# Kernel tuning notes

Measured on AMD Instinct MI355X. Metric: run time of the kernel, lower is better.

Reference implementation:

```python
import jax, jax.numpy as jnp
import numpy as np

ALPHA = 0.2  # LeakyReLU negative slope


def setup_inputs() -> dict:
    key = jax.random.key(0)
    k1, k2, k3, k4 = jax.random.split(key, 4)
    bs, n, fin = 8, 1024, 256
    heads, fo = 8, 64
    h = jax.random.normal(k1, (bs, n, fin), dtype=jnp.float32)
    adj = jax.random.randint(k2, (bs, n, n), 0, 2, dtype=jnp.int32)
    # W stored as [in_features, heads*out] so Wh = h @ W (same math as torch Linear)
    W = jax.random.normal(k3, (fin, heads * fo), dtype=jnp.float32) * 0.1
    a = jax.random.normal(k4, (heads, 2 * fo), dtype=jnp.float32) * 0.1
    return {"h": h, "adj": adj, "W": W, "a": a}


def reference(h, adj, W, a):
    bs, n, _ = h.shape
    heads, two_fo = a.shape
    fo = two_fo // 2
    # Wh: [bs, n, heads, fo]
    Wh = (h @ W).reshape(bs, n, heads, fo)
    a_src, a_dst = a[:, :fo], a[:, fo:]
    # Additive attention decomposed: e[b,h,i,j] = leaky_relu(src[b,h,i] + dst[b,h,j])
    e_src = jnp.einsum('bnhf,hf->bhn', Wh, a_src)  # [bs, heads, n]
    e_dst = jnp.einsum('bnhf,hf->bhn', Wh, a_dst)
    e = e_src[:, :, :, None] + e_dst[:, :, None, :]  # [bs, heads, n, n]
    e = jnp.where(e > 0, e, ALPHA * e)  # LeakyReLU
    e = jnp.where(adj[:, None, :, :] == 0, -jnp.inf, e)
    attn = jax.nn.softmax(e, axis=-1)  # [bs, heads, n, n]
    # h_prime[b,i,h,f] = sum_j attn[b,h,i,j] * Wh[b,j,h,f]
    h_prime = jnp.einsum('bhij,bjhf->bihf', attn, Wh)
    return h_prime.reshape(bs, n, heads * fo)
```

## Files before the change

kernel.cpp:

```cpp
#include <hip/hip_runtime.h>
#include <hip/hip_bf16.h>
#include <math.h>

#define BS 8
#define NN 1024
#define FIN 256
#define HEADS 8
#define FO 64
#define NH (HEADS*FO)
static constexpr float ALPHA = 0.2f;
static constexpr float LOG2E = 1.4426950408889634f;

typedef short bf16x8 __attribute__((ext_vector_type(8)));
typedef float f32x4  __attribute__((ext_vector_type(4)));
typedef unsigned short u16;
typedef unsigned u32;
typedef u16 u16x4v __attribute__((ext_vector_type(4)));
typedef u16 u16x8v __attribute__((ext_vector_type(8)));

__device__ __forceinline__ u16 f2b(float x) {
    __hip_bfloat16 b = __float2bfloat16(x);
    return *reinterpret_cast<u16*>(&b);
}
__device__ __forceinline__ float fexp2(float x) {
#if __has_builtin(__builtin_amdgcn_exp2f)
    return __builtin_amdgcn_exp2f(x);
#else
    float r; asm("v_exp_f32 %0, %1" : "=v"(r) : "v"(x)); return r;
#endif
}
__device__ __forceinline__ void gload_lds16(const void* g, void* l) {
    __builtin_amdgcn_global_load_lds(
        (const __attribute__((address_space(1))) unsigned int*)g,
        (__attribute__((address_space(3))) unsigned int*)l, 16, 0, 0);
}

__global__ __launch_bounds__(256) void prep_misc(const float* __restrict__ h,
                                                 const int* __restrict__ adj,
                                                 const float* __restrict__ W,
                                                 u16* __restrict__ hb,
                                                 u16* __restrict__ WbT,
                                                 u32* __restrict__ bits) {
    const int bid = blockIdx.x;
    const int t = threadIdx.x;
    if (bid < 8192) {
        const int lane = t & 63;
        const size_t e0 = ((size_t)bid * 256 + t) * 4;
        const int4 v = *reinterpret_cast<const int4*>(adj + e0);
        u32 x = (v.x ? 1u : 0u) | (v.y ? 2u : 0u) | (v.z ? 4u : 0u) | (v.w ? 8u : 0u);
        {   const u32 r = (u32)__shfl_xor((int)x, 1);
            const int sh = (lane & 1) * 4;  x = (x << sh) | (r << (4 - sh)); }
        {   const u32 r = (u32)__shfl_xor((int)x, 2);
            const int sh = (lane & 2) * 4;  x = (x << sh) | (r << (8 - sh)); }
        {   const u32 r = (u32)__shfl_xor((int)x, 4);
            const int sh = (lane & 4) * 4;  x = (x << sh) | (r << (16 - sh)); }
        if ((lane & 7) == 0) bits[e0 >> 5] = x;
    } else if (bid < 9216) {
        const int i = ((bid - 8192) * 256 + t) * 8;
        const float4 v0 = *reinterpret_cast<const float4*>(h + i);
        const float4 v1 = *reinterpret_cast<const float4*>(h + i + 4);
        u16x8v o;
        o[0]=f2b(v0.x); o[1]=f2b(v0.y); o[2]=f2b(v0.z); o[3]=f2b(v0.w);
        o[4]=f2b(v1.x); o[5]=f2b(v1.y); o[6]=f2b(v1.z); o[7]=f2b(v1.w);
        *reinterpret_cast<u16x8v*>(hb + i) = o;
    } else {
        __shared__ float T[64][65];
        const int bb = bid - 9216;
        const int hh = bb & 7;
        const int n0 = hh * 64, k0 = (bb >> 3) * 64;
        const int r4 = t >> 6, c = t & 63;
        #pragma unroll
        for (int p = 0; p < 16; ++p) {
            const int r = p * 4 + r4;
            T[r][c] = W[(size_t)(k0 + r) * NH + n0 + c];
        }
        __syncthreads();
        #pragma unroll
        for (int p = 0; p < 16; ++p) {
            const int r = p * 4 + r4;
            WbT[(size_t)(n0 + r) * FIN + k0 + c] = f2b(T[c][r]);
        }
    }
}

__global__ __launch_bounds__(256) void gemm_whT(const u16* __restrict__ hb,
                                                const u16* __restrict__ WbT,
                                                const float* __restrict__ avec,
                                                u16* __restrict__ WhT,
                                                float* __restrict__ esrc,
                                                float* __restrict__ edst) {
    __shared__ u16 Al[2][64 * 64];
    __shared__ u16 Bl[2][64 * 64];
    const int t = threadIdx.x, wv = t >> 6, lane = t & 63;
    const int g = lane >> 4, l15 = lane & 15;
    const int lid = (blockIdx.x & 7) * 128 + (blockIdx.x >> 3);
    const int m0 = (lid >> 3) * 64;
    const int h  = lid & 7;
    const int lr = lane >> 3;
    const int sch = (lane & 7) ^ lr;
    const int bh = (m0 >> 10) * HEADS + h;

    f32x4 acc[4] = {};

    auto stageA = [&](int buf, int k0) {
        #pragma unroll
        for (int c = 0; c < 2; ++c) {
            const int rowb = wv * 16 + c * 8;
            gload_lds16(hb + (size_t)(m0 + rowb + lr) * FIN + k0 + sch * 8,
                        &Al[buf][rowb * 64]);
        }
    };
    auto stageB = [&](int buf, int k0) {
        #pragma unroll
        for (int c = 0; c < 2; ++c) {
            const int rowb = wv * 16 + c * 8;
            gload_lds16(WbT + (size_t)(h * 64 + rowb + lr) * FIN + k0 + sch * 8,
                        &Bl[buf][rowb * 64]);
        }
    };

    stageA(0, 0); stageB(0, 0);
    __syncthreads();
    for (int kt = 0; kt < 4; ++kt) {
        const int buf = kt & 1;
        if (kt < 3) { stageA(buf ^ 1, (kt + 1) * 64); stageB(buf ^ 1, (kt + 1) * 64); }
        #pragma unroll
        for (int ks = 0; ks < 2; ++ks) {
            const int ch = (ks * 4 + g) ^ (l15 & 7);
            const bf16x8 afr = *reinterpret_cast<const bf16x8*>(
                &Al[buf][(wv * 16 + l15) * 64 + ch * 8]);
            #pragma unroll
            for (int n = 0; n < 4; ++n) {
                const bf16x8 bfr = *reinterpret_cast<const bf16x8*>(
                    &Bl[buf][(n * 16 + l15) * 64 + ch * 8]);
                acc[n] = __builtin_amdgcn_mfma_f32_16x16x32_bf16(afr, bfr, acc[n], 0, 0, 0);
            }
        }
        __syncthreads();
    }

    {
        float as_[4], ad_[4];
        #pragma unroll
        for (int n = 0; n < 4; ++n) {
            as_[n] = avec[h * 128 + n * 16 + l15] * LOG2E;
            ad_[n] = avec[h * 128 + 64 + n * 16 + l15] * LOG2E;
        }
        #pragma unroll
        for (int r = 0; r < 4; ++r) {
            float ps = acc[0][r] * as_[0] + acc[1][r] * as_[1]
                     + acc[2][r] * as_[2] + acc[3][r] * as_[3];
            float pd = acc[0][r] * ad_[0] + acc[1][r] * ad_[1]
                     + acc[2][r] * ad_[2] + acc[3][r] * ad_[3];
            #pragma unroll
            for (int off = 1; off < 16; off <<= 1) {
                ps += __shfl_xor(ps, off);
                pd += __shfl_xor(pd, off);
            }
            if (l15 == 0) {
                const int i = (m0 + wv * 16 + g * 4 + r) & (NN - 1);
                esrc[(size_t)bh * NN + i] = ps;
                edst[(size_t)bh * NN + i] = pd;
            }
        }
    }

    u16* scr = &Al[0][0];
    #pragma unroll
    for (int n = 0; n < 4; ++n) {
        u16x4v pk;
        #pragma unroll
        for (int r = 0; r < 4; ++r) pk[r] = f2b(acc[n][r]);
        *reinterpret_cast<u16x4v*>(&scr[(n * 16 + l15) * 72 + wv * 16 + g * 4]) = pk;
    }
    __syncthreads();
    const int il0 = m0 & (NN - 1);
    const int f = t >> 2, q = t & 3;
    const u16x8v v0 = *reinterpret_cast<const u16x8v*>(&scr[f * 72 + q * 16]);
    const u16x8v v1 = *reinterpret_cast<const u16x8v*>(&scr[f * 72 + q * 16 + 8]);
    u16* dst = &WhT[((size_t)bh * 64 + f) * NN + il0 + q * 16];
    *reinterpret_cast<u16x8v*>(dst)     = v0;
    *reinterpret_cast<u16x8v*>(dst + 8) = v1;
}

__global__ __launch_bounds__(128, 4) void attn_pv(const u32* __restrict__ bits,
                                                  const u16* __restrict__ WhT,
                                                  const float* __restrict__ esrc,
                                                  const float* __restrict__ edst,
                                                  float* __restrict__ out) {
    __shared__ u16 Bs[2][64 * 64];
    const int t = threadIdx.x, wv = t >> 6, lane = t & 63;
    const int g = lane >> 4, l15 = lane & 15;
    const int lr = lane >> 3, sch = (lane & 7) ^ lr;

    const int lid = (blockIdx.x & 7) * 256 + (blockIdx.x >> 3);
    const int it = lid & 31, h = (lid >> 5) & 7, b = lid >> 8;
    const int i0 = it * 32;
    const int bh = b * HEADS + h;
    const int rowi = i0 + wv * 16 + l15;

    const float es = esrc[(size_t)bh * NN + rowi];
    const u16*  whb = WhT + (size_t)bh * 64 * NN;
    const float* ed = edst + (size_t)bh * NN + 8 * g;
    const u32*  bitrow = bits + (size_t)(b * NN + rowi) * 32;

    auto stageB = [&](int buf, int j0) {
        #pragma unroll
        for (int c = 0; c < 4; ++c) {
            const int fb = wv * 32 + c * 8;
            gload_lds16(whb + (size_t)(fb + lr) * NN + j0 + sch * 8,
                        &Bs[buf][fb * 64]);
        }
    };

    stageB(0, 0);
    float4 pe0 = *(const float4*)(ed);
    float4 pe1 = *(const float4*)(ed + 4);
    u32    pw  = bitrow[0];
    __syncthreads();

    f32x4 acc[4] = {};
    f32x4 dsum = {};
    bf16x8 ones;
    #pragma unroll
    for (int q = 0; q < 8; ++q) ones[q] = (short)0x3F80;

    for (int tt = 0; tt < 16; ++tt) {
        const int buf = tt & 1;
        if (tt < 15) stageB(buf ^ 1, (tt + 1) * 64);
        #pragma unroll
        for (int ks = 0; ks < 2; ++ks) {
            const int s = tt * 2 + ks;
            const float4 e0 = pe0, e1 = pe1;
            const u32 word = pw;
            if (s < 31) {
                pe0 = *(const float4*)(ed + (s + 1) * 32);
                pe1 = *(const float4*)(ed + (s + 1) * 32 + 4);
                pw  = bitrow[s + 1];
            }
            const int chb = ((ks * 4 + g) ^ (l15 & 7)) * 8;
            const bf16x8 v0 = *(const bf16x8*)(&Bs[buf][(0 * 16 + l15) * 64 + chb]);
            const bf16x8 v1 = *(const bf16x8*)(&Bs[buf][(1 * 16 + l15) * 64 + chb]);
            const bf16x8 v2 = *(const bf16x8*)(&Bs[buf][(2 * 16 + l15) * 64 + chb]);
            const bf16x8 v3 = *(const bf16x8*)(&Bs[buf][(3 * 16 + l15) * 64 + chb]);

            const u32 byte_ = (word >> (8 * g)) & 0xffu;
            float ps[8];
            {
                float sv;
                sv = es + e0.x; sv = fmaxf(sv, ALPHA * sv); sv = (byte_ & 1u)        ? sv : -1e30f; ps[0] = fexp2(sv);
                sv = es + e0.y; sv = fmaxf(sv, ALPHA * sv); sv = ((byte_ >> 1) & 1u) ? sv : -1e30f; ps[1] = fexp2(sv);
                sv = es + e0.z; sv = fmaxf(sv, ALPHA * sv); sv = ((byte_ >> 2) & 1u) ? sv : -1e30f; ps[2] = fexp2(sv);
                sv = es + e0.w; sv = fmaxf(sv, ALPHA * sv); sv = ((byte_ >> 3) & 1u) ? sv : -1e30f; ps[3] = fexp2(sv);
                sv = es + e1.x; sv = fmaxf(sv, ALPHA * sv); sv = ((byte_ >> 4) & 1u) ? sv : -1e30f; ps[4] = fexp2(sv);
                sv = es + e1.y; sv = fmaxf(sv, ALPHA * sv); sv = ((byte_ >> 5) & 1u) ? sv : -1e30f; ps[5] = fexp2(sv);
                sv = es + e1.z; sv = fmaxf(sv, ALPHA * sv); sv = ((byte_ >> 6) & 1u) ? sv : -1e30f; ps[6] = fexp2(sv);
                sv = es + e1.w; sv = fmaxf(sv, ALPHA * sv); sv = ((byte_ >> 7) & 1u) ? sv : -1e30f; ps[7] = fexp2(sv);
            }
            union { u32 u[4]; bf16x8 v; } af;
            #pragma unroll
            for (int qp = 0; qp < 4; ++qp) {
                union { __hip_bfloat162 b2; u32 w; } cv;
                cv.b2 = __float22bfloat162_rn(make_float2(ps[2*qp], ps[2*qp+1]));
                af.u[qp] = cv.w;
            }
            acc[0] = __builtin_amdgcn_mfma_f32_16x16x32_bf16(af.v, v0, acc[0], 0, 0, 0);
            acc[1] = __builtin_amdgcn_mfma_f32_16x16x32_bf16(af.v, v1, acc[1], 0, 0, 0);
            acc[2] = __builtin_amdgcn_mfma_f32_16x16x32_bf16(af.v, v2, acc[2], 0, 0, 0);
            acc[3] = __builtin_amdgcn_mfma_f32_16x16x32_bf16(af.v, v3, acc[3], 0, 0, 0);
            dsum   = __builtin_amdgcn_mfma_f32_16x16x32_bf16(af.v, ones, dsum, 0, 0, 0);
        }
        if (tt < 15) __syncthreads();
    }

    float inv[4];
    #pragma unroll
    for (int r = 0; r < 4; ++r) inv[r] = 1.0f / dsum[r];
    #pragma unroll
    for (int n = 0; n < 4; ++n)
        #pragma unroll
        for (int r = 0; r < 4; ++r) {
            const int io = i0 + wv * 16 + g * 4 + r;
            out[(size_t)(b * NN + io) * NH + h * 64 + n * 16 + l15] =
                acc[n][r] * inv[r];
        }
}

extern "C" void kernel_launch(void* const* d_in, const int* in_sizes, int n_in,
                              void* d_out, int out_size, void* d_ws, size_t ws_size,
                              hipStream_t stream) {
    const float* h   = (const float*)d_in[0];
    const int*   adj = (const int*)  d_in[1];
    const float* W   = (const float*)d_in[2];
    const float* a   = (const float*)d_in[3];
    float* out = (float*)d_out;

    char* p = (char*)d_ws;
    u16*   hb   = (u16*)p;   p += (size_t)BS * NN * FIN * 2;
    u16*   WbT  = (u16*)p;   p += (size_t)NH * FIN * 2;
    u16*   WhT  = (u16*)p;   p += (size_t)BS * HEADS * FO * NN * 2;
    float* esrc = (float*)p; p += (size_t)BS * HEADS * NN * 4;
    float* edst = (float*)p; p += (size_t)BS * HEADS * NN * 4;
    u32*   bits = (u32*)p;

    prep_misc<<<9248, 256, 0, stream>>>(h, adj, W, hb, WbT, bits);
    gemm_whT <<<1024, 256, 0, stream>>>(hb, WbT, a, WhT, esrc, edst);
    attn_pv  <<<2048, 128, 0, stream>>>(bits, WhT, esrc, edst, out);
}
```

Before: 53.34 us.

## Deepen prefetch of edge scores and mask bits, relax barrier waitcnt, raise MFMA priority

```diff
diff --git a/kernel.cpp b/kernel.cpp
--- a/kernel.cpp
+++ b/kernel.cpp
@@ -214,9 +214,14 @@
     };
 
     stageB(0, 0);
-    float4 pe0 = *(const float4*)(ed);
-    float4 pe1 = *(const float4*)(ed + 4);
-    u32    pw  = bitrow[0];
+    float4 peA[2], peB[2];
+    u32    pwS[2];
+    #pragma unroll
+    for (int s = 0; s < 2; ++s) {
+        peA[s] = *(const float4*)(ed + s * 32);
+        peB[s] = *(const float4*)(ed + s * 32 + 4);
+        pwS[s] = bitrow[s];
+    }
     __syncthreads();
 
     f32x4 acc[4] = {};
@@ -227,16 +232,20 @@
 
     for (int tt = 0; tt < 16; ++tt) {
         const int buf = tt & 1;
-        if (tt < 15) stageB(buf ^ 1, (tt + 1) * 64);
+        const bool more = (tt < 15);
+        if (more) {
+            stageB(buf ^ 1, (tt + 1) * 64);
+            asm volatile("" ::: "memory");
+        }
         #pragma unroll
         for (int ks = 0; ks < 2; ++ks) {
             const int s = tt * 2 + ks;
-            const float4 e0 = pe0, e1 = pe1;
-            const u32 word = pw;
-            if (s < 31) {
-                pe0 = *(const float4*)(ed + (s + 1) * 32);
-                pe1 = *(const float4*)(ed + (s + 1) * 32 + 4);
-                pw  = bitrow[s + 1];
+            const float4 e0 = peA[ks], e1 = peB[ks];
+            const u32 word = pwS[ks];
+            if (more) {
+                peA[ks] = *(const float4*)(ed + (s + 2) * 32);
+                peB[ks] = *(const float4*)(ed + (s + 2) * 32 + 4);
+                pwS[ks] = bitrow[s + 2];
             }
             const int chb = ((ks * 4 + g) ^ (l15 & 7)) * 8;
             const bf16x8 v0 = *(const bf16x8*)(&Bs[buf][(0 * 16 + l15) * 64 + chb]);
@@ -264,13 +273,18 @@
                 cv.b2 = __float22bfloat162_rn(make_float2(ps[2*qp], ps[2*qp+1]));
                 af.u[qp] = cv.w;
             }
+            __builtin_amdgcn_s_setprio(1);
             acc[0] = __builtin_amdgcn_mfma_f32_16x16x32_bf16(af.v, v0, acc[0], 0, 0, 0);
             acc[1] = __builtin_amdgcn_mfma_f32_16x16x32_bf16(af.v, v1, acc[1], 0, 0, 0);
             acc[2] = __builtin_amdgcn_mfma_f32_16x16x32_bf16(af.v, v2, acc[2], 0, 0, 0);
             acc[3] = __builtin_amdgcn_mfma_f32_16x16x32_bf16(af.v, v3, acc[3], 0, 0, 0);
             dsum   = __builtin_amdgcn_mfma_f32_16x16x32_bf16(af.v, ones, dsum, 0, 0, 0);
-        }
-        if (tt < 15) __syncthreads();
+            __builtin_amdgcn_s_setprio(0);
+        }
+        if (more) {
+            asm volatile("s_waitcnt vmcnt(6)" ::: "memory");
+            __builtin_amdgcn_s_barrier();
+        }
     }
 
     float inv[4];
```

After: 51.35 us. -3.7%, faster.
